# Performance work log

Hardware: AMD Instinct MI355X
Metric: run time of the kernel (lower is better)

Reference implementation:

```python
import jax, jax.numpy as jnp
import numpy as np

N = 100000      # nodes
E = 1600000     # edges
F_IN = 128      # num_feat
H = 128         # hidden_dim
EMB = 64        # node_embedding_dim
HL = 256        # hidden_dim_linear


def setup_inputs() -> dict:
    key = jax.random.key(0)
    ks = jax.random.split(key, 12)
    def w(k, fan_in, shape):
        return jax.random.normal(k, shape, dtype=jnp.float32) / np.sqrt(fan_in)
    x = jax.random.normal(ks[0], (N, F_IN), dtype=jnp.float32)
    edge_index = jax.random.randint(ks[1], (2, E), 0, N, dtype=jnp.int32)
    return {
        "x": x,
        "edge_index": edge_index,
        "W0": w(ks[2], F_IN, (F_IN, H)), "b0": jnp.zeros((H,), jnp.float32),
        "W1": w(ks[3], H, (H, H)),       "b1": jnp.zeros((H,), jnp.float32),
        "W2": w(ks[4], H, (H, EMB)),     "b2": jnp.zeros((EMB,), jnp.float32),
        "lw1": w(ks[5], 2 * EMB, (2 * EMB, HL)), "lb1": jnp.zeros((HL,), jnp.float32),
        "lw2": w(ks[6], HL, (HL, 1)),            "lb2": jnp.zeros((1,), jnp.float32),
    }


def _gcn_forward(x, edge_index, W0, b0, W1, b1, W2, b2, lw1, lb1, lw2, lb2):
    src, dst = edge_index[0], edge_index[1]
    # add self loops (PyG GCNConv default) -- shared across layers
    loop = jnp.arange(N, dtype=src.dtype)
    s = jnp.concatenate([src, loop])
    d = jnp.concatenate([dst, loop])
    # symmetric normalization: deg counts incoming edges incl. self loop (>=1)
    deg = jax.ops.segment_sum(jnp.ones_like(d, dtype=x.dtype), d, num_segments=N)
    norm = jax.lax.rsqrt(deg[s] * deg[d])  # [E+N]

    def conv(h, W, b):
        hw = h @ W                                   # small GEMM [N, out]
        msg = hw[s] * norm[:, None]                  # gather + scale [E+N, out]
        agg = jax.ops.segment_sum(msg, d, num_segments=N)
        return agg + b

    z = jax.nn.relu(conv(x, W0, b0))
    z = jax.nn.relu(conv(z, W1, b1))
    z = jax.nn.relu(conv(z, W2, b2))                 # [N, EMB]  (dropout: eval mode, no-op)

    # edge classifier: gather both endpoints, cat, MLP, sigmoid
    h = jnp.concatenate([z[src], z[dst]], axis=1)    # [E, 2*EMB]
    h = jax.nn.relu(h @ lw1 + lb1)
    return jax.nn.sigmoid(h @ lw2 + lb2)             # [E, 1]


def reference(x, edge_index, W0, b0, W1, b1, W2, b2, lw1, lb1, lw2, lb2):
    return _gcn_forward(x, edge_index, W0, b0, W1, b1, W2, b2, lw1, lb1, lw2, lb2)
```

## Files before the change

### kernel.cpp

```cpp
#include <hip/hip_runtime.h>

#define NNODES 100000
#define NEDGES 1600000
#define NBLK 391
#define NSLICE 8
#define SLICEW 12500

typedef __attribute__((ext_vector_type(8))) short bf16x8;
typedef __attribute__((ext_vector_type(4))) float f32x4;

__device__ __forceinline__ unsigned short f2bf(float f) {
  unsigned int u = __float_as_uint(f);
  u = (u + 0x7FFFu + ((u >> 16) & 1u)) >> 16;
  return (unsigned short)u;
}
__device__ __forceinline__ float bf2f(unsigned short h) {
  return __uint_as_float(((unsigned int)h) << 16);
}

__device__ __forceinline__ unsigned int pk_add_f16(unsigned int a, unsigned int b) {
  unsigned int r;
  asm("v_pk_add_f16 %0, %1, %2" : "=v"(r) : "v"(a), "v"(b));
  return r;
}
__device__ __forceinline__ unsigned int pk_max0_f16(unsigned int a, unsigned int z) {
  unsigned int r;
  asm("v_pk_max_f16 %0, %1, %2" : "=v"(r) : "v"(a), "v"(z));
  return r;
}
__device__ __forceinline__ float dot2_f16(unsigned int a, unsigned int b, float c) {
  float r;
  asm("v_dot2_f32_f16 %0, %1, %2, %3" : "=v"(r) : "v"(a), "v"(b), "v"(c));
  return r;
}

__global__ void count_kernel(const int* __restrict__ dst, int* __restrict__ cntD) {
  int slice = blockIdx.x & (NSLICE - 1);
  int e = (blockIdx.x >> 3) * 256 + threadIdx.x;
  if (e >= NEDGES) return;
  int d = dst[e];
  int lo = slice * SLICEW;
  if (d >= lo && d < lo + SLICEW) atomicAdd(&cntD[d], 1);
}

__global__ void scanA_kernel(const int* __restrict__ cntD, int* __restrict__ blockSum) {
  __shared__ int sh[256];
  int v = blockIdx.x * 256 + threadIdx.x;
  sh[threadIdx.x] = (v < NNODES) ? cntD[v] : 0;
  __syncthreads();
  for (int off = 128; off; off >>= 1) {
    if (threadIdx.x < off) sh[threadIdx.x] += sh[threadIdx.x + off];
    __syncthreads();
  }
  if (threadIdx.x == 0) blockSum[blockIdx.x] = sh[0];
}

__global__ void scanB_kernel(int* __restrict__ blockSum) {
  int lane = threadIdx.x;
  int carry = 0;
  for (int base = 0; base < NBLK; base += 64) {
    int i = base + lane;
    int c = (i < NBLK) ? blockSum[i] : 0;
    int pre = c;
#pragma unroll
    for (int off = 1; off < 64; off <<= 1) {
      int t = __shfl_up(pre, off);
      if (lane >= off) pre += t;
    }
    int tot = __shfl(pre, 63);
    if (i < NBLK) blockSum[i] = carry + pre - c;
    carry += tot;
  }
}

__global__ void scanC_kernel(const int* __restrict__ cntD, const int* __restrict__ blockSum,
                             int* __restrict__ startD, int* __restrict__ curD,
                             float* __restrict__ dis) {
  __shared__ int sh[256];
  int tid = threadIdx.x;
  int v = blockIdx.x * 256 + tid;
  int c = (v < NNODES) ? cntD[v] : 0;
  sh[tid] = c;
  __syncthreads();
  for (int off = 1; off < 256; off <<= 1) {
    int t = (tid >= off) ? sh[tid - off] : 0;
    __syncthreads();
    sh[tid] += t;
    __syncthreads();
  }
  if (v < NNODES) {
    int s = blockSum[blockIdx.x] + sh[tid] - c;
    startD[v] = s;
    curD[v] = s;
    dis[v] = rsqrtf((float)(c + 1));
  }
}

__global__ void fill_kernel(const int* __restrict__ src, const int* __restrict__ dst,
                            int* __restrict__ curD, int2* __restrict__ csrPair) {
  int slice = blockIdx.x & (NSLICE - 1);
  int e = (blockIdx.x >> 3) * 256 + threadIdx.x;
  if (e >= NEDGES) return;
  int d = dst[e];
  int lo = slice * SLICEW;
  if (d < lo || d >= lo + SLICEW) return;
  int s = src[e];
  int pd = atomicAdd(&curD[d], 1);
  csrPair[pd] = make_int2(s, e);
}

template <int K, int HOUT>
__global__ void pack_w_kernel(const float* __restrict__ W, unsigned short* __restrict__ Wp) {
  int idx = blockIdx.x * 256 + threadIdx.x;
  if (idx < K * HOUT) {
    int k = idx / HOUT, c = idx - k * HOUT;
    Wp[((size_t)((k >> 5) * HOUT + c)) * 32 + (k & 31)] = f2bf(W[idx]);
  }
}

__global__ void pack_lw1_kernel(const float* __restrict__ lw1, const float* __restrict__ lb1,
                                const float* __restrict__ lw2,
                                unsigned short* __restrict__ Wp, float* __restrict__ biasAB,
                                unsigned int* __restrict__ wh) {
  int idx = blockIdx.x * 256 + threadIdx.x;
  if (idx < 64 * 512) {
    int k = idx / 512, c = idx - k * 512;
    float v = (c < 256) ? lw1[k * 256 + c] : lw1[(64 + k) * 256 + (c - 256)];
    Wp[((size_t)((k >> 5) * 512 + c)) * 32 + (k & 31)] = f2bf(v);
  }
  if (idx < 512) biasAB[idx] = (idx < 256) ? lb1[idx] : 0.0f;
  if (idx < 128) {
    _Float16 lo = (_Float16)lw2[idx * 2];
    _Float16 hi = (_Float16)lw2[idx * 2 + 1];
    unsigned short ulo = __builtin_bit_cast(unsigned short, lo);
    unsigned short uhi = __builtin_bit_cast(unsigned short, hi);
    wh[idx] = (unsigned int)ulo | ((unsigned int)uhi << 16);
  }
}

template <int K, int HOUT, bool SCALE, bool BIAS, bool F32IN, bool F16OUT>
__global__ __launch_bounds__(256)
void mgemm_kernel(const void* __restrict__ Xhi_v, const void* __restrict__ Xlo_v,
                  const unsigned short* __restrict__ Wp, const float* __restrict__ dis,
                  const float* __restrict__ bias, void* __restrict__ outv) {
  constexpr int KC = K / 32;
  const int tid = threadIdx.x;
  const int wave = tid >> 6;
  const int lane = tid & 63;
  const int lrow = lane & 15;
  const int lsub = lane >> 4;
  const int rowBase = blockIdx.x * 64 + wave * 16;
  int arow = rowBase + lrow;
  if (arow > NNODES - 1) arow = NNODES - 1;
  bf16x8 ahi[KC], alo[KC];
  if constexpr (F32IN) {
    const float* xf = (const float*)Xhi_v;
#pragma unroll
    for (int kc = 0; kc < KC; ++kc) {
      float4 v0 = *(const float4*)&xf[(size_t)arow * K + kc * 32 + lsub * 8];
      float4 v1 = *(const float4*)&xf[(size_t)arow * K + kc * 32 + lsub * 8 + 4];
      float fv[8] = {v0.x, v0.y, v0.z, v0.w, v1.x, v1.y, v1.z, v1.w};
#pragma unroll
      for (int i = 0; i < 8; ++i) {
        unsigned short h = f2bf(fv[i]);
        ahi[kc][i] = (short)h;
        alo[kc][i] = (short)f2bf(fv[i] - bf2f(h));
      }
    }
  } else {
    const unsigned short* Xhi = (const unsigned short*)Xhi_v;
    const unsigned short* Xlo = (const unsigned short*)Xlo_v;
#pragma unroll
    for (int kc = 0; kc < KC; ++kc) {
      ahi[kc] = *(const bf16x8*)&Xhi[(size_t)arow * K + kc * 32 + lsub * 8];
      alo[kc] = *(const bf16x8*)&Xlo[(size_t)arow * K + kc * 32 + lsub * 8];
    }
  }
  int orow[4];
  float dis4[4];
#pragma unroll
  for (int i = 0; i < 4; ++i) {
    orow[i] = rowBase + lsub * 4 + i;
    int rc = orow[i] < NNODES ? orow[i] : NNODES - 1;
    dis4[i] = SCALE ? dis[rc] : 1.0f;
  }
  for (int ct = 0; ct < HOUT / 16; ++ct) {
    int c = ct * 16 + lrow;
    f32x4 acc = {0.f, 0.f, 0.f, 0.f};
#pragma unroll
    for (int kc = 0; kc < KC; ++kc) {
      bf16x8 b = *(const bf16x8*)&Wp[((size_t)(kc * HOUT + c)) * 32 + lsub * 8];
      acc = __builtin_amdgcn_mfma_f32_16x16x32_bf16(ahi[kc], b, acc, 0, 0, 0);
      acc = __builtin_amdgcn_mfma_f32_16x16x32_bf16(alo[kc], b, acc, 0, 0, 0);
    }
    float bb = BIAS ? bias[c] : 0.0f;
#pragma unroll
    for (int i = 0; i < 4; ++i) {
      if (orow[i] < NNODES) {
        float v = acc[i];
        if (SCALE) v *= dis4[i];
        if (BIAS) v += bb;
        if constexpr (F16OUT) {
          ((_Float16*)outv)[(size_t)orow[i] * HOUT + c] = (_Float16)v;
        } else {
          ((unsigned short*)outv)[(size_t)orow[i] * HOUT + c] = f2bf(v);
        }
      }
    }
  }
}

template <int HOUT>
__global__ __launch_bounds__(256)
void agg_kernel(const unsigned short* __restrict__ hws, const int2* __restrict__ csrPair,
                const int* __restrict__ startA, const int* __restrict__ cnt,
                const float* __restrict__ dis, const float* __restrict__ bias,
                unsigned short* __restrict__ outHi, unsigned short* __restrict__ outLo) {
  int gid = blockIdx.x * 256 + threadIdx.x;
  int v = gid >> 6;
  int lane = gid & 63;
  constexpr int PER = HOUT / 64;
  float acc0 = 0.0f, acc1 = 0.0f;
  if constexpr (PER == 2) {
    unsigned int o = *(const unsigned int*)&hws[(size_t)v * HOUT + lane * 2];
    acc0 = __uint_as_float(o << 16);
    acc1 = __uint_as_float(o & 0xffff0000u);
  } else {
    acc0 = bf2f(hws[(size_t)v * HOUT + lane]);
  }
  int s0 = startA[v], c = cnt[v];
  for (int base = 0; base < c; base += 64) {
    int rem = c - base;
    int m = rem < 64 ? rem : 64;
    int idx = 0;
    if (lane < m) idx = csrPair[s0 + base + lane].x;
    int j = 0;
    for (; j + 4 <= m; j += 4) {
      int u0 = __shfl(idx, j);
      int u1 = __shfl(idx, j + 1);
      int u2 = __shfl(idx, j + 2);
      int u3 = __shfl(idx, j + 3);
      if constexpr (PER == 2) {
        unsigned int r0 = *(const unsigned int*)&hws[(size_t)u0 * HOUT + lane * 2];
        unsigned int r1 = *(const unsigned int*)&hws[(size_t)u1 * HOUT + lane * 2];
        unsigned int r2 = *(const unsigned int*)&hws[(size_t)u2 * HOUT + lane * 2];
        unsigned int r3 = *(const unsigned int*)&hws[(size_t)u3 * HOUT + lane * 2];
        acc0 += __uint_as_float(r0 << 16) + __uint_as_float(r1 << 16) +
                __uint_as_float(r2 << 16) + __uint_as_float(r3 << 16);
        acc1 += __uint_as_float(r0 & 0xffff0000u) + __uint_as_float(r1 & 0xffff0000u) +
                __uint_as_float(r2 & 0xffff0000u) + __uint_as_float(r3 & 0xffff0000u);
      } else {
        float r0 = bf2f(hws[(size_t)u0 * HOUT + lane]);
        float r1 = bf2f(hws[(size_t)u1 * HOUT + lane]);
        float r2 = bf2f(hws[(size_t)u2 * HOUT + lane]);
        float r3 = bf2f(hws[(size_t)u3 * HOUT + lane]);
        acc0 += (r0 + r1) + (r2 + r3);
      }
    }
    for (; j < m; ++j) {
      int u = __shfl(idx, j);
      if constexpr (PER == 2) {
        unsigned int r = *(const unsigned int*)&hws[(size_t)u * HOUT + lane * 2];
        acc0 += __uint_as_float(r << 16);
        acc1 += __uint_as_float(r & 0xffff0000u);
      } else {
        acc0 += bf2f(hws[(size_t)u * HOUT + lane]);
      }
    }
  }
  float d = dis[v];
  if constexpr (PER == 2) {
    float o0 = fmaf(d, acc0, bias[lane * 2]);
    float o1 = fmaf(d, acc1, bias[lane * 2 + 1]);
    o0 = o0 > 0.0f ? o0 : 0.0f;
    o1 = o1 > 0.0f ? o1 : 0.0f;
    ushort2 h, l;
    h.x = f2bf(o0); l.x = f2bf(o0 - bf2f(h.x));
    h.y = f2bf(o1); l.y = f2bf(o1 - bf2f(h.y));
    *(ushort2*)&outHi[(size_t)v * HOUT + lane * 2] = h;
    *(ushort2*)&outLo[(size_t)v * HOUT + lane * 2] = l;
  } else {
    float o0 = fmaf(d, acc0, bias[lane]);
    o0 = o0 > 0.0f ? o0 : 0.0f;
    unsigned short h = f2bf(o0);
    outHi[(size_t)v * HOUT + lane] = h;
    outLo[(size_t)v * HOUT + lane] = f2bf(o0 - bf2f(h));
  }
}

__global__ __launch_bounds__(256)
void edge_kernel(const unsigned int* __restrict__ AB32,
                 const int2* __restrict__ csrPair,
                 const int* __restrict__ startD, const int* __restrict__ cntD,
                 const unsigned int* __restrict__ wh, const float* __restrict__ lb2,
                 float* __restrict__ out) {
  int gid = blockIdx.x * 256 + threadIdx.x;
  int v = gid >> 6;
  int lane = gid & 63;
  int sub = lane & 15;
  unsigned int zero = 0u;
  unsigned int bu[8], wu[8];
  {
    const unsigned int* Brow = AB32 + (size_t)v * 256 + 128 + sub * 8;
    uint4 b0 = *(const uint4*)Brow;
    uint4 b1 = *(const uint4*)(Brow + 4);
    bu[0] = b0.x; bu[1] = b0.y; bu[2] = b0.z; bu[3] = b0.w;
    bu[4] = b1.x; bu[5] = b1.y; bu[6] = b1.z; bu[7] = b1.w;
    const unsigned int* W = wh + sub * 8;
    uint4 w0 = *(const uint4*)W;
    uint4 w1 = *(const uint4*)(W + 4);
    wu[0] = w0.x; wu[1] = w0.y; wu[2] = w0.z; wu[3] = w0.w;
    wu[4] = w1.x; wu[5] = w1.y; wu[6] = w1.z; wu[7] = w1.w;
  }
  float lb = lb2[0];

  int s0 = startD[v], c = cntD[v];
  for (int base = 0; base < c; base += 64) {
    int rem = c - base;
    int m = rem < 64 ? rem : 64;
    int sj = 0, ej = 0;
    if (lane < m) {
      int2 p = csrPair[s0 + base + lane];
      sj = p.x; ej = p.y;
    }
    int g = lane >> 4;
    for (int j = 0; j < m; j += 8) {
      int ls0 = j + g, ls1 = j + 4 + g;
      int l0 = ls0 < m ? ls0 : m - 1;
      int l1 = ls1 < m ? ls1 : m - 1;
      int sA = __shfl(sj, l0);
      int eA = __shfl(ej, l0);
      int sB = __shfl(sj, l1);
      int eB = __shfl(ej, l1);
      const unsigned int* ArowA = AB32 + (size_t)(unsigned)sA * 256 + sub * 8;
      const unsigned int* ArowB = AB32 + (size_t)(unsigned)sB * 256 + sub * 8;
      uint4 a00 = *(const uint4*)ArowA;
      uint4 a01 = *(const uint4*)(ArowA + 4);
      uint4 a10 = *(const uint4*)ArowB;
      uint4 a11 = *(const uint4*)(ArowB + 4);
      unsigned int au0[8] = {a00.x, a00.y, a00.z, a00.w, a01.x, a01.y, a01.z, a01.w};
      unsigned int au1[8] = {a10.x, a10.y, a10.z, a10.w, a11.x, a11.y, a11.z, a11.w};
      float acc0 = 0.f, acc1 = 0.f;
#pragma unroll
      for (int i = 0; i < 8; ++i) {
        unsigned int h0 = pk_max0_f16(pk_add_f16(au0[i], bu[i]), zero);
        acc0 = dot2_f16(h0, wu[i], acc0);
        unsigned int h1 = pk_max0_f16(pk_add_f16(au1[i], bu[i]), zero);
        acc1 = dot2_f16(h1, wu[i], acc1);
      }
      acc0 += __shfl_xor(acc0, 1);
      acc0 += __shfl_xor(acc0, 2);
      acc0 += __shfl_xor(acc0, 4);
      acc0 += __shfl_xor(acc0, 8);
      acc1 += __shfl_xor(acc1, 1);
      acc1 += __shfl_xor(acc1, 2);
      acc1 += __shfl_xor(acc1, 4);
      acc1 += __shfl_xor(acc1, 8);
      if (ls0 < m && sub == 0) out[eA] = 1.0f / (1.0f + expf(-(acc0 + lb)));
      if (ls1 < m && sub == 0) out[eB] = 1.0f / (1.0f + expf(-(acc1 + lb)));
    }
  }
}

extern "C" void kernel_launch(void* const* d_in, const int* in_sizes, int n_in,
                              void* d_out, int out_size, void* d_ws, size_t ws_size,
                              hipStream_t stream) {
  const float* x   = (const float*)d_in[0];
  const int*   ei  = (const int*)d_in[1];
  const float* W0  = (const float*)d_in[2];
  const float* b0  = (const float*)d_in[3];
  const float* W1  = (const float*)d_in[4];
  const float* b1  = (const float*)d_in[5];
  const float* W2  = (const float*)d_in[6];
  const float* b2  = (const float*)d_in[7];
  const float* lw1 = (const float*)d_in[8];
  const float* lb1 = (const float*)d_in[9];
  const float* lw2 = (const float*)d_in[10];
  const float* lb2 = (const float*)d_in[11];
  float* out = (float*)d_out;
  const int* src = ei;
  const int* dst = ei + NEDGES;

  char* ws = (char*)d_ws;
  size_t off = 0;
  auto alloc = [&](size_t bytes) -> void* {
    void* p = ws + off;
    off += (bytes + 255) & ~(size_t)255;
    return p;
  };
  int*   cntD   = (int*)alloc((size_t)NNODES * 4);
  int*   startD = (int*)alloc((size_t)NNODES * 4);
  int*   curD   = (int*)alloc((size_t)NNODES * 4);
  float* dis    = (float*)alloc((size_t)NNODES * 4);
  int*   blockSum = (int*)alloc((size_t)NBLK * 4);
  int2*  csrPair= (int2*)alloc((size_t)NEDGES * 8);
  unsigned short* P16  = (unsigned short*)alloc((size_t)NNODES * 128 * 2);
  unsigned short* XQhi = (unsigned short*)alloc((size_t)NNODES * 128 * 2);
  unsigned short* XQlo = (unsigned short*)alloc((size_t)NNODES * 128 * 2);
  void*           AB   = alloc((size_t)NNODES * 512 * 2);
  unsigned short* Wp0  = (unsigned short*)alloc((size_t)128 * 128 * 2);
  unsigned short* Wp1  = (unsigned short*)alloc((size_t)128 * 128 * 2);
  unsigned short* Wp2  = (unsigned short*)alloc((size_t)128 * 64 * 2);
  unsigned short* WpE  = (unsigned short*)alloc((size_t)64 * 512 * 2);
  float* biasAB = (float*)alloc(512 * 4);
  unsigned int* wh = (unsigned int*)alloc(128 * 4);

  const int EB8 = NSLICE * ((NEDGES + 255) / 256);

  hipMemsetAsync(cntD, 0, (size_t)NNODES * 4, stream);
  count_kernel<<<EB8, 256, 0, stream>>>(dst, cntD);
  scanA_kernel<<<NBLK, 256, 0, stream>>>(cntD, blockSum);
  scanB_kernel<<<1, 64, 0, stream>>>(blockSum);
  scanC_kernel<<<NBLK, 256, 0, stream>>>(cntD, blockSum, startD, curD, dis);
  fill_kernel<<<EB8, 256, 0, stream>>>(src, dst, curD, csrPair);

  pack_w_kernel<128, 128><<<64, 256, 0, stream>>>(W0, Wp0);
  pack_w_kernel<128, 128><<<64, 256, 0, stream>>>(W1, Wp1);
  pack_w_kernel<128, 64><<<32, 256, 0, stream>>>(W2, Wp2);
  pack_lw1_kernel<<<128, 256, 0, stream>>>(lw1, lb1, lw2, WpE, biasAB, wh);

  const int GB = (NNODES + 63) / 64;
  const int AB_ = (NNODES * 64) / 256;

  mgemm_kernel<128, 128, true, false, true, false><<<GB, 256, 0, stream>>>(x, nullptr, Wp0, dis, nullptr, P16);
  agg_kernel<128><<<AB_, 256, 0, stream>>>(P16, csrPair, startD, cntD, dis, b0, XQhi, XQlo);
  mgemm_kernel<128, 128, true, false, false, false><<<GB, 256, 0, stream>>>(XQhi, XQlo, Wp1, dis, nullptr, P16);
  agg_kernel<128><<<AB_, 256, 0, stream>>>(P16, csrPair, startD, cntD, dis, b1, XQhi, XQlo);
  mgemm_kernel<128, 64, true, false, false, false><<<GB, 256, 0, stream>>>(XQhi, XQlo, Wp2, dis, nullptr, P16);
  agg_kernel<64><<<AB_, 256, 0, stream>>>(P16, csrPair, startD, cntD, dis, b2, XQhi, XQlo);

  mgemm_kernel<64, 512, false, true, false, true><<<GB, 256, 0, stream>>>(XQhi, XQlo, WpE, nullptr, biasAB, AB);

  edge_kernel<<<AB_, 256, 0, stream>>>((const unsigned int*)AB, csrPair, startD, cntD, wh, lb2, out);
}
```

Measured before the change: 594.8 us.

## Merge preprocessing launches into fused kernels and deepen agg unroll to eight

Several small kernels are merged into fewer launches. The edge count and all weight-packing work go into one kernel, the dis computation moves into scanA, and the first GEMM runs in the same launch as the scanC prefix pass. The count kernel drops its 8-way dst slicing and issues atomics over the whole range in one pass, which may add atomic contention or hurt L2 locality. The aggregation loop gains an 8-wide unrolled gather stage, giving more memory-level parallelism at the cost of more registers.

```diff
diff --git a/kernel.cpp b/kernel.cpp
--- a/kernel.cpp
+++ b/kernel.cpp
@@ -5,6 +5,8 @@
 #define NBLK 391
 #define NSLICE 8
 #define SLICEW 12500
+#define CNTB 6250
+#define GB0 1563
 
 typedef __attribute__((ext_vector_type(8))) short bf16x8;
 typedef __attribute__((ext_vector_type(4))) float f32x4;
@@ -34,19 +36,57 @@
   return r;
 }
 
-__global__ void count_kernel(const int* __restrict__ dst, int* __restrict__ cntD) {
-  int slice = blockIdx.x & (NSLICE - 1);
-  int e = (blockIdx.x >> 3) * 256 + threadIdx.x;
-  if (e >= NEDGES) return;
-  int d = dst[e];
-  int lo = slice * SLICEW;
-  if (d >= lo && d < lo + SLICEW) atomicAdd(&cntD[d], 1);
-}
-
-__global__ void scanA_kernel(const int* __restrict__ cntD, int* __restrict__ blockSum) {
+__global__ __launch_bounds__(256)
+void k1_kernel(const int* __restrict__ dst, int* __restrict__ cntD,
+               const float* __restrict__ W0, const float* __restrict__ W1,
+               const float* __restrict__ W2, const float* __restrict__ lw1,
+               const float* __restrict__ lb1, const float* __restrict__ lw2,
+               unsigned short* __restrict__ Wp0, unsigned short* __restrict__ Wp1,
+               unsigned short* __restrict__ Wp2, unsigned short* __restrict__ WpE,
+               float* __restrict__ biasAB, unsigned int* __restrict__ wh) {
+  int b = blockIdx.x;
+  int tid = threadIdx.x;
+  if (b < CNTB) {
+    int e = b * 256 + tid;
+    if (e < NEDGES) atomicAdd(&cntD[dst[e]], 1);
+    return;
+  }
+  int bb = b - CNTB;
+  if (bb < 64) {
+    int idx = bb * 256 + tid;
+    int k = idx >> 7, c = idx & 127;
+    Wp0[((size_t)((k >> 5) * 128 + c)) * 32 + (k & 31)] = f2bf(W0[idx]);
+  } else if (bb < 128) {
+    int idx = (bb - 64) * 256 + tid;
+    int k = idx >> 7, c = idx & 127;
+    Wp1[((size_t)((k >> 5) * 128 + c)) * 32 + (k & 31)] = f2bf(W1[idx]);
+  } else if (bb < 160) {
+    int idx = (bb - 128) * 256 + tid;
+    int k = idx >> 6, c = idx & 63;
+    Wp2[((size_t)((k >> 5) * 64 + c)) * 32 + (k & 31)] = f2bf(W2[idx]);
+  } else {
+    int idx = (bb - 160) * 256 + tid;
+    int k = idx >> 9, c = idx & 511;
+    float v = (c < 256) ? lw1[k * 256 + c] : lw1[(64 + k) * 256 + (c - 256)];
+    WpE[((size_t)((k >> 5) * 512 + c)) * 32 + (k & 31)] = f2bf(v);
+    if (idx < 512) biasAB[idx] = (idx < 256) ? lb1[idx] : 0.0f;
+    if (idx < 128) {
+      _Float16 lo = (_Float16)lw2[idx * 2];
+      _Float16 hi = (_Float16)lw2[idx * 2 + 1];
+      unsigned short ulo = __builtin_bit_cast(unsigned short, lo);
+      unsigned short uhi = __builtin_bit_cast(unsigned short, hi);
+      wh[idx] = (unsigned int)ulo | ((unsigned int)uhi << 16);
+    }
+  }
+}
+
+__global__ void scanA_kernel(const int* __restrict__ cntD, int* __restrict__ blockSum,
+                             float* __restrict__ dis) {
   __shared__ int sh[256];
   int v = blockIdx.x * 256 + threadIdx.x;
-  sh[threadIdx.x] = (v < NNODES) ? cntD[v] : 0;
+  int c = (v < NNODES) ? cntD[v] : 0;
+  if (v < NNODES) dis[v] = rsqrtf((float)(c + 1));
+  sh[threadIdx.x] = c;
   __syncthreads();
   for (int off = 128; off; off >>= 1) {
     if (threadIdx.x < off) sh[threadIdx.x] += sh[threadIdx.x + off];
@@ -73,12 +113,101 @@
   }
 }
 
-__global__ void scanC_kernel(const int* __restrict__ cntD, const int* __restrict__ blockSum,
-                             int* __restrict__ startD, int* __restrict__ curD,
-                             float* __restrict__ dis) {
+template <int K, int HOUT, bool SCALE, bool BIAS, bool F32IN, bool F16OUT>
+__device__ __forceinline__ void mgemm_body(int bid, const void* __restrict__ Xhi_v,
+                                           const void* __restrict__ Xlo_v,
+                                           const unsigned short* __restrict__ Wp,
+                                           const float* __restrict__ dis,
+                                           const float* __restrict__ bias,
+                                           void* __restrict__ outv) {
+  constexpr int KC = K / 32;
+  const int tid = threadIdx.x;
+  const int wave = tid >> 6;
+  const int lane = tid & 63;
+  const int lrow = lane & 15;
+  const int lsub = lane >> 4;
+  const int rowBase = bid * 64 + wave * 16;
+  int arow = rowBase + lrow;
+  if (arow > NNODES - 1) arow = NNODES - 1;
+  bf16x8 ahi[KC], alo[KC];
+  if constexpr (F32IN) {
+    const float* xf = (const float*)Xhi_v;
+#pragma unroll
+    for (int kc = 0; kc < KC; ++kc) {
+      float4 v0 = *(const float4*)&xf[(size_t)arow * K + kc * 32 + lsub * 8];
+      float4 v1 = *(const float4*)&xf[(size_t)arow * K + kc * 32 + lsub * 8 + 4];
+      float fv[8] = {v0.x, v0.y, v0.z, v0.w, v1.x, v1.y, v1.z, v1.w};
+#pragma unroll
+      for (int i = 0; i < 8; ++i) {
+        unsigned short h = f2bf(fv[i]);
+        ahi[kc][i] = (short)h;
+        alo[kc][i] = (short)f2bf(fv[i] - bf2f(h));
+      }
+    }
+  } else {
+    const unsigned short* Xhi = (const unsigned short*)Xhi_v;
+    const unsigned short* Xlo = (const unsigned short*)Xlo_v;
+#pragma unroll
+    for (int kc = 0; kc < KC; ++kc) {
+      ahi[kc] = *(const bf16x8*)&Xhi[(size_t)arow * K + kc * 32 + lsub * 8];
+      alo[kc] = *(const bf16x8*)&Xlo[(size_t)arow * K + kc * 32 + lsub * 8];
+    }
+  }
+  int orow[4];
+  float dis4[4];
+#pragma unroll
+  for (int i = 0; i < 4; ++i) {
+    orow[i] = rowBase + lsub * 4 + i;
+    int rc = orow[i] < NNODES ? orow[i] : NNODES - 1;
+    dis4[i] = SCALE ? dis[rc] : 1.0f;
+  }
+  for (int ct = 0; ct < HOUT / 16; ++ct) {
+    int c = ct * 16 + lrow;
+    f32x4 acc = {0.f, 0.f, 0.f, 0.f};
+#pragma unroll
+    for (int kc = 0; kc < KC; ++kc) {
+      bf16x8 b = *(const bf16x8*)&Wp[((size_t)(kc * HOUT + c)) * 32 + lsub * 8];
+      acc = __builtin_amdgcn_mfma_f32_16x16x32_bf16(ahi[kc], b, acc, 0, 0, 0);
+      acc = __builtin_amdgcn_mfma_f32_16x16x32_bf16(alo[kc], b, acc, 0, 0, 0);
+    }
+    float bb = BIAS ? bias[c] : 0.0f;
+#pragma unroll
+    for (int i = 0; i < 4; ++i) {
+      if (orow[i] < NNODES) {
+        float v = acc[i];
+        if (SCALE) v *= dis4[i];
+        if (BIAS) v += bb;
+        if constexpr (F16OUT) {
+          ((_Float16*)outv)[(size_t)orow[i] * HOUT + c] = (_Float16)v;
+        } else {
+          ((unsigned short*)outv)[(size_t)orow[i] * HOUT + c] = f2bf(v);
+        }
+      }
+    }
+  }
+}
+
+template <int K, int HOUT, bool SCALE, bool BIAS, bool F32IN, bool F16OUT>
+__global__ __launch_bounds__(256)
+void mgemm_kernel(const void* __restrict__ Xhi_v, const void* __restrict__ Xlo_v,
+                  const unsigned short* __restrict__ Wp, const float* __restrict__ dis,
+                  const float* __restrict__ bias, void* __restrict__ outv) {
+  mgemm_body<K, HOUT, SCALE, BIAS, F32IN, F16OUT>(blockIdx.x, Xhi_v, Xlo_v, Wp, dis, bias, outv);
+}
+
+__global__ __launch_bounds__(256)
+void mg0_scanC_kernel(const float* __restrict__ x, const unsigned short* __restrict__ Wp0,
+                      const float* __restrict__ dis, unsigned short* __restrict__ P16,
+                      const int* __restrict__ cntD, const int* __restrict__ blockSum,
+                      int* __restrict__ startD, int* __restrict__ curD) {
+  if (blockIdx.x < GB0) {
+    mgemm_body<128, 128, true, false, true, false>(blockIdx.x, x, nullptr, Wp0, dis, nullptr, P16);
+    return;
+  }
   __shared__ int sh[256];
+  int bid = blockIdx.x - GB0;
   int tid = threadIdx.x;
-  int v = blockIdx.x * 256 + tid;
+  int v = bid * 256 + tid;
   int c = (v < NNODES) ? cntD[v] : 0;
   sh[tid] = c;
   __syncthreads();
@@ -89,10 +218,9 @@
     __syncthreads();
   }
   if (v < NNODES) {
-    int s = blockSum[blockIdx.x] + sh[tid] - c;
+    int s = blockSum[bid] + sh[tid] - c;
     startD[v] = s;
     curD[v] = s;
-    dis[v] = rsqrtf((float)(c + 1));
   }
 }
 
@@ -107,107 +235,6 @@
   int s = src[e];
   int pd = atomicAdd(&curD[d], 1);
   csrPair[pd] = make_int2(s, e);
-}
-
-template <int K, int HOUT>
-__global__ void pack_w_kernel(const float* __restrict__ W, unsigned short* __restrict__ Wp) {
-  int idx = blockIdx.x * 256 + threadIdx.x;
-  if (idx < K * HOUT) {
-    int k = idx / HOUT, c = idx - k * HOUT;
-    Wp[((size_t)((k >> 5) * HOUT + c)) * 32 + (k & 31)] = f2bf(W[idx]);
-  }
-}
-
-__global__ void pack_lw1_kernel(const float* __restrict__ lw1, const float* __restrict__ lb1,
-                                const float* __restrict__ lw2,
-                                unsigned short* __restrict__ Wp, float* __restrict__ biasAB,
-                                unsigned int* __restrict__ wh) {
-  int idx = blockIdx.x * 256 + threadIdx.x;
-  if (idx < 64 * 512) {
-    int k = idx / 512, c = idx - k * 512;
-    float v = (c < 256) ? lw1[k * 256 + c] : lw1[(64 + k) * 256 + (c - 256)];
-    Wp[((size_t)((k >> 5) * 512 + c)) * 32 + (k & 31)] = f2bf(v);
-  }
-  if (idx < 512) biasAB[idx] = (idx < 256) ? lb1[idx] : 0.0f;
-  if (idx < 128) {
-    _Float16 lo = (_Float16)lw2[idx * 2];
-    _Float16 hi = (_Float16)lw2[idx * 2 + 1];
-    unsigned short ulo = __builtin_bit_cast(unsigned short, lo);
-    unsigned short uhi = __builtin_bit_cast(unsigned short, hi);
-    wh[idx] = (unsigned int)ulo | ((unsigned int)uhi << 16);
-  }
-}
-
-template <int K, int HOUT, bool SCALE, bool BIAS, bool F32IN, bool F16OUT>
-__global__ __launch_bounds__(256)
-void mgemm_kernel(const void* __restrict__ Xhi_v, const void* __restrict__ Xlo_v,
-                  const unsigned short* __restrict__ Wp, const float* __restrict__ dis,
-                  const float* __restrict__ bias, void* __restrict__ outv) {
-  constexpr int KC = K / 32;
-  const int tid = threadIdx.x;
-  const int wave = tid >> 6;
-  const int lane = tid & 63;
-  const int lrow = lane & 15;
-  const int lsub = lane >> 4;
-  const int rowBase = blockIdx.x * 64 + wave * 16;
-  int arow = rowBase + lrow;
-  if (arow > NNODES - 1) arow = NNODES - 1;
-  bf16x8 ahi[KC], alo[KC];
-  if constexpr (F32IN) {
-    const float* xf = (const float*)Xhi_v;
-#pragma unroll
-    for (int kc = 0; kc < KC; ++kc) {
-      float4 v0 = *(const float4*)&xf[(size_t)arow * K + kc * 32 + lsub * 8];
-      float4 v1 = *(const float4*)&xf[(size_t)arow * K + kc * 32 + lsub * 8 + 4];
-      float fv[8] = {v0.x, v0.y, v0.z, v0.w, v1.x, v1.y, v1.z, v1.w};
-#pragma unroll
-      for (int i = 0; i < 8; ++i) {
-        unsigned short h = f2bf(fv[i]);
-        ahi[kc][i] = (short)h;
-        alo[kc][i] = (short)f2bf(fv[i] - bf2f(h));
-      }
-    }
-  } else {
-    const unsigned short* Xhi = (const unsigned short*)Xhi_v;
-    const unsigned short* Xlo = (const unsigned short*)Xlo_v;
-#pragma unroll
-    for (int kc = 0; kc < KC; ++kc) {
-      ahi[kc] = *(const bf16x8*)&Xhi[(size_t)arow * K + kc * 32 + lsub * 8];
-      alo[kc] = *(const bf16x8*)&Xlo[(size_t)arow * K + kc * 32 + lsub * 8];
-    }
-  }
-  int orow[4];
-  float dis4[4];
-#pragma unroll
-  for (int i = 0; i < 4; ++i) {
-    orow[i] = rowBase + lsub * 4 + i;
-    int rc = orow[i] < NNODES ? orow[i] : NNODES - 1;
-    dis4[i] = SCALE ? dis[rc] : 1.0f;
-  }
-  for (int ct = 0; ct < HOUT / 16; ++ct) {
-    int c = ct * 16 + lrow;
-    f32x4 acc = {0.f, 0.f, 0.f, 0.f};
-#pragma unroll
-    for (int kc = 0; kc < KC; ++kc) {
-      bf16x8 b = *(const bf16x8*)&Wp[((size_t)(kc * HOUT + c)) * 32 + lsub * 8];
-      acc = __builtin_amdgcn_mfma_f32_16x16x32_bf16(ahi[kc], b, acc, 0, 0, 0);
-      acc = __builtin_amdgcn_mfma_f32_16x16x32_bf16(alo[kc], b, acc, 0, 0, 0);
-    }
-    float bb = BIAS ? bias[c] : 0.0f;
-#pragma unroll
-    for (int i = 0; i < 4; ++i) {
-      if (orow[i] < NNODES) {
-        float v = acc[i];
-        if (SCALE) v *= dis4[i];
-        if (BIAS) v += bb;
-        if constexpr (F16OUT) {
-          ((_Float16*)outv)[(size_t)orow[i] * HOUT + c] = (_Float16)v;
-        } else {
-          ((unsigned short*)outv)[(size_t)orow[i] * HOUT + c] = f2bf(v);
-        }
-      }
-    }
-  }
 }
 
 template <int HOUT>
@@ -235,6 +262,44 @@
     int idx = 0;
     if (lane < m) idx = csrPair[s0 + base + lane].x;
     int j = 0;
+    for (; j + 8 <= m; j += 8) {
+      int u0 = __shfl(idx, j);
+      int u1 = __shfl(idx, j + 1);
+      int u2 = __shfl(idx, j + 2);
+      int u3 = __shfl(idx, j + 3);
+      int u4 = __shfl(idx, j + 4);
+      int u5 = __shfl(idx, j + 5);
+      int u6 = __shfl(idx, j + 6);
+      int u7 = __shfl(idx, j + 7);
+      if constexpr (PER == 2) {
+        unsigned int r0 = *(const unsigned int*)&hws[(size_t)u0 * HOUT + lane * 2];
+        unsigned int r1 = *(const unsigned int*)&hws[(size_t)u1 * HOUT + lane * 2];
+        unsigned int r2 = *(const unsigned int*)&hws[(size_t)u2 * HOUT + lane * 2];
+        unsigned int r3 = *(const unsigned int*)&hws[(size_t)u3 * HOUT + lane * 2];
+        unsigned int r4 = *(const unsigned int*)&hws[(size_t)u4 * HOUT + lane * 2];
+        unsigned int r5 = *(const unsigned int*)&hws[(size_t)u5 * HOUT + lane * 2];
+        unsigned int r6 = *(const unsigned int*)&hws[(size_t)u6 * HOUT + lane * 2];
+        unsigned int r7 = *(const unsigned int*)&hws[(size_t)u7 * HOUT + lane * 2];
+        acc0 += (__uint_as_float(r0 << 16) + __uint_as_float(r1 << 16)) +
+                (__uint_as_float(r2 << 16) + __uint_as_float(r3 << 16)) +
+                (__uint_as_float(r4 << 16) + __uint_as_float(r5 << 16)) +
+                (__uint_as_float(r6 << 16) + __uint_as_float(r7 << 16));
+        acc1 += (__uint_as_float(r0 & 0xffff0000u) + __uint_as_float(r1 & 0xffff0000u)) +
+                (__uint_as_float(r2 & 0xffff0000u) + __uint_as_float(r3 & 0xffff0000u)) +
+                (__uint_as_float(r4 & 0xffff0000u) + __uint_as_float(r5 & 0xffff0000u)) +
+                (__uint_as_float(r6 & 0xffff0000u) + __uint_as_float(r7 & 0xffff0000u));
+      } else {
+        float r0 = bf2f(hws[(size_t)u0 * HOUT + lane]);
+        float r1 = bf2f(hws[(size_t)u1 * HOUT + lane]);
+        float r2 = bf2f(hws[(size_t)u2 * HOUT + lane]);
+        float r3 = bf2f(hws[(size_t)u3 * HOUT + lane]);
+        float r4 = bf2f(hws[(size_t)u4 * HOUT + lane]);
+        float r5 = bf2f(hws[(size_t)u5 * HOUT + lane]);
+        float r6 = bf2f(hws[(size_t)u6 * HOUT + lane]);
+        float r7 = bf2f(hws[(size_t)u7 * HOUT + lane]);
+        acc0 += ((r0 + r1) + (r2 + r3)) + ((r4 + r5) + (r6 + r7));
+      }
+    }
     for (; j + 4 <= m; j += 4) {
       int u0 = __shfl(idx, j);
       int u1 = __shfl(idx, j + 1);
@@ -405,31 +470,24 @@
   float* biasAB = (float*)alloc(512 * 4);
   unsigned int* wh = (unsigned int*)alloc(128 * 4);
 
-  const int EB8 = NSLICE * ((NEDGES + 255) / 256);
+  const int EB8 = NSLICE * CNTB;
+  const int AB_ = (NNODES * 64) / 256;
 
   hipMemsetAsync(cntD, 0, (size_t)NNODES * 4, stream);
-  count_kernel<<<EB8, 256, 0, stream>>>(dst, cntD);
-  scanA_kernel<<<NBLK, 256, 0, stream>>>(cntD, blockSum);
+  k1_kernel<<<CNTB + 288, 256, 0, stream>>>(dst, cntD, W0, W1, W2, lw1, lb1, lw2,
+                                            Wp0, Wp1, Wp2, WpE, biasAB, wh);
+  scanA_kernel<<<NBLK, 256, 0, stream>>>(cntD, blockSum, dis);
   scanB_kernel<<<1, 64, 0, stream>>>(blockSum);
-  scanC_kernel<<<NBLK, 256, 0, stream>>>(cntD, blockSum, startD, curD, dis);
+  mg0_scanC_kernel<<<GB0 + NBLK, 256, 0, stream>>>(x, Wp0, dis, P16, cntD, blockSum, startD, curD);
   fill_kernel<<<EB8, 256, 0, stream>>>(src, dst, curD, csrPair);
 
-  pack_w_kernel<128, 128><<<64, 256, 0, stream>>>(W0, Wp0);
-  pack_w_kernel<128, 128><<<64, 256, 0, stream>>>(W1, Wp1);
-  pack_w_kernel<128, 64><<<32, 256, 0, stream>>>(W2, Wp2);
-  pack_lw1_kernel<<<128, 256, 0, stream>>>(lw1, lb1, lw2, WpE, biasAB, wh);
-
-  const int GB = (NNODES + 63) / 64;
-  const int AB_ = (NNODES * 64) / 256;
-
-  mgemm_kernel<128, 128, true, false, true, false><<<GB, 256, 0, stream>>>(x, nullptr, Wp0, dis, nullptr, P16);
   agg_kernel<128><<<AB_, 256, 0, stream>>>(P16, csrPair, startD, cntD, dis, b0, XQhi, XQlo);
-  mgemm_kernel<128, 128, true, false, false, false><<<GB, 256, 0, stream>>>(XQhi, XQlo, Wp1, dis, nullptr, P16);
+  mgemm_kernel<128, 128, true, false, false, false><<<GB0, 256, 0, stream>>>(XQhi, XQlo, Wp1, dis, nullptr, P16);
   agg_kernel<128><<<AB_, 256, 0, stream>>>(P16, csrPair, startD, cntD, dis, b1, XQhi, XQlo);
-  mgemm_kernel<128, 64, true, false, false, false><<<GB, 256, 0, stream>>>(XQhi, XQlo, Wp2, dis, nullptr, P16);
+  mgemm_kernel<128, 64, true, false, false, false><<<GB0, 256, 0, stream>>>(XQhi, XQlo, Wp2, dis, nullptr, P16);
   agg_kernel<64><<<AB_, 256, 0, stream>>>(P16, csrPair, startD, cntD, dis, b2, XQhi, XQlo);
 
-  mgemm_kernel<64, 512, false, true, false, true><<<GB, 256, 0, stream>>>(XQhi, XQlo, WpE, nullptr, biasAB, AB);
+  mgemm_kernel<64, 512, false, true, false, true><<<GB0, 256, 0, stream>>>(XQhi, XQlo, WpE, nullptr, biasAB, AB);
 
   edge_kernel<<<AB_, 256, 0, stream>>>((const unsigned int*)AB, csrPair, startD, cntD, wh, lb2, out);
 }
```

Result: faster. 580.8 us (-2.3%).
